# Performance work log

Measured on AMD Instinct MI355X. Metric: run time of the kernel, lower is better.

The kernel has to match this reference:

```python
import jax, jax.numpy as jnp
import numpy as np

B, S, T = 32, 512, 20      # sentences, tokens/sentence, chars/word
N_CHARS = 128              # embedding rows = N_CHARS + 1 (0 is pad)
D = 128                    # char_dim
H = 256                    # char_lstm_dim


def _gru_last_state(x_tnd, mask_tn, Wk, Wr, b):
    """Keras GRU (reset_after=True, gate order z,r,h) over time-major input.
    x_tnd: [T, N, D], mask_tn: [T, N] bool. Masked steps pass state through.
    Returns final hidden state [N, H]."""
    h_dim = Wr.shape[0]
    b_in, b_rec = b[0], b[1]

    def step(h, inp):
        x, m = inp
        xg = x @ Wk + b_in            # [N, 3H]
        hg = h @ Wr + b_rec           # [N, 3H]
        xz, xr, xh = jnp.split(xg, 3, axis=-1)
        hz, hr, hh = jnp.split(hg, 3, axis=-1)
        z = jax.nn.sigmoid(xz + hz)
        r = jax.nn.sigmoid(xr + hr)
        hc = jnp.tanh(xh + r * hh)
        hn = z * h + (1.0 - z) * hc
        hn = jnp.where(m[:, None], hn, h)
        return hn, None

    h0 = jnp.zeros((x_tnd.shape[1], h_dim), dtype=x_tnd.dtype)
    hT, _ = jax.lax.scan(step, h0, (x_tnd, mask_tn))
    return hT


def setup_inputs() -> dict:
    key = jax.random.key(0)
    ks = jax.random.split(key, 8)
    inputs = jax.random.randint(ks[0], (B, S, T), 0, N_CHARS + 1, dtype=jnp.int32)
    sc = 0.05
    emb = jax.random.normal(ks[1], (N_CHARS + 1, D), dtype=jnp.float32) * sc
    Wk_f = jax.random.normal(ks[2], (D, 3 * H), dtype=jnp.float32) * sc
    Wr_f = jax.random.normal(ks[3], (H, 3 * H), dtype=jnp.float32) * sc
    b_f = jnp.zeros((2, 3 * H), dtype=jnp.float32)
    Wk_b = jax.random.normal(ks[4], (D, 3 * H), dtype=jnp.float32) * sc
    Wr_b = jax.random.normal(ks[5], (H, 3 * H), dtype=jnp.float32) * sc
    b_b = jnp.zeros((2, 3 * H), dtype=jnp.float32)
    return {"inputs": inputs, "emb": emb, "Wk_f": Wk_f, "Wr_f": Wr_f,
            "b_f": b_f, "Wk_b": Wk_b, "Wr_b": Wr_b, "b_b": b_b}


def reference(inputs, emb, Wk_f, Wr_f, b_f, Wk_b, Wr_b, b_b):
    bsz, seq, wlen = inputs.shape
    h_dim = Wr_f.shape[0]
    flat = inputs.reshape(bsz * seq, wlen)           # [N, T]
    mask = flat != 0                                 # [N, T] (0 = pad)
    x = emb[flat]                                    # [N, T, D]
    x_t = jnp.transpose(x, (1, 0, 2))                # [T, N, D]
    m_t = mask.T                                     # [T, N]
    h_fwd = _gru_last_state(x_t, m_t, Wk_f, Wr_f, b_f)
    # Bidirectional: backward layer sees the reversed sequence + reversed mask
    h_bwd = _gru_last_state(x_t[::-1], m_t[::-1], Wk_b, Wr_b, b_b)
    out = jnp.concatenate([h_fwd, h_bwd], axis=-1)   # [N, 2H]
    return out.reshape(bsz, seq, 2 * h_dim)
```

## Files before the change

kernel.cpp:

```cpp
#include <hip/hip_runtime.h>
#include <hip/hip_bf16.h>

#define TS 20
#define DNUM 128
#define NWORDS 16384
#define NBLK 256

typedef __attribute__((ext_vector_type(8))) short s8v;
typedef __attribute__((ext_vector_type(4))) float f4v;

#define L2E 1.4426950408889634f

__device__ __forceinline__ unsigned short bf16_rne(float f) {
  union { float f; unsigned u; } x; x.f = f;
  unsigned r = x.u + 0x7fffu + ((x.u >> 16) & 1u);
  return (unsigned short)(r >> 16);
}

__global__ void build_tab(const float* __restrict__ emb,
                          const float* __restrict__ wkF, const float* __restrict__ bF,
                          const float* __restrict__ wkB, const float* __restrict__ bB,
                          float* __restrict__ tab2, float* __restrict__ tabh) {
  int gid = blockIdx.x * 256 + threadIdx.x;
  if (gid >= 2 * 129 * 768) return;
  int dir = gid / (129 * 768);
  int rem = gid - dir * (129 * 768);
  int c = rem / 768, j = rem - (rem / 768) * 768;
  int g = j >> 8, u = j & 255;
  const float* Wk = dir ? wkB : wkF;
  const float* bb = dir ? bB : bF;
  float s = bb[j];
  const float* er = emb + c * DNUM;
  #pragma unroll 4
  for (int d = 0; d < DNUM; ++d) s = fmaf(er[d], Wk[d * 768 + j], s);
  if (g < 2) tab2[(((size_t)dir * 129 + c) * 256 + u) * 2 + g] = -L2E * (s + bb[768 + j]);
  else       tabh[((size_t)dir * 129 + c) * 256 + u] = 2.f * L2E * s;
}

__global__ void pack_wr(const float* __restrict__ wrF, const float* __restrict__ wrB,
                        uint4* __restrict__ wp) {
  int gid = blockIdx.x * 256 + threadIdx.x;
  if (gid >= 2 * 48 * 8 * 64) return;
  int dir = gid / (48 * 8 * 64);
  int rem = gid - dir * (48 * 8 * 64);
  int ct = rem / (8 * 64);
  int kk = (rem / 64) & 7;
  int lane = rem & 63;
  const float* Wr = dir ? wrB : wrF;
  int n = ct * 16 + (lane & 15);
  int k0 = kk * 32 + (lane >> 4) * 8;
  const float sc = (ct >> 4) == 2 ? (2.f * L2E) : (-L2E);
  union { unsigned short v[8]; uint4 q; } u;
  #pragma unroll
  for (int e = 0; e < 8; ++e) u.v[e] = bf16_rne(sc * Wr[(k0 + e) * 768 + n]);
  wp[gid] = u.q;
}

__global__ __launch_bounds__(512, 2) void gru_main(
    const int* __restrict__ chars, const float* __restrict__ tab2,
    const float* __restrict__ tabh, const uint4* __restrict__ wrp,
    const float* __restrict__ bf_, const float* __restrict__ bb_,
    float* __restrict__ out) {
  const int bid = blockIdx.x;
  const int dir = bid >> 7;
  const int wslot = bid & 127;
  const float2* T2 = (const float2*)tab2 + (size_t)dir * 129 * 256;
  const float*  TH = tabh + (size_t)dir * 129 * 256;
  const uint4* WP = wrp + dir * (48 * 8 * 64);
  const float* brec = (dir ? bb_ : bf_) + 768;

  const int tid = threadIdx.x;
  const int w = tid >> 6, lane = tid & 63;
  const int lr = lane >> 4, lc = lane & 15;
  const int u0 = w * 32 + lc, u1 = u0 + 16;

  __shared__ uint4 bhl[8192];
  __shared__ unsigned short hbf[16][264];
  __shared__ int sch[16 * TS];

  for (int i = tid; i < 8192; i += 512) bhl[i] = WP[16384 + i];

  uint4 Wz[2][8], Wrr[2][8];
  #pragma unroll
  for (int ct = 0; ct < 2; ++ct)
    #pragma unroll
    for (int kk = 0; kk < 8; ++kk) {
      Wz[ct][kk]  = WP[((w * 2 + ct) * 8 + kk) * 64 + lane];
      Wrr[ct][kk] = WP[((16 + w * 2 + ct) * 8 + kk) * 64 + lane];
    }

  float brh[2];
  brh[0] = 2.f * L2E * brec[512 + u0];
  brh[1] = 2.f * L2E * brec[512 + u1];

  #pragma unroll 1
  for (int grp = 0; grp < 8; ++grp) {
    const int word0 = wslot * 128 + grp * 16;

    for (int i = tid; i < 16 * 264 / 2; i += 512) ((unsigned*)&hbf[0][0])[i] = 0;
    for (int i = tid; i < 16 * TS; i += 512) sch[i] = chars[word0 * TS + i];

    float h[2][4];
    #pragma unroll
    for (int ct = 0; ct < 2; ++ct)
      #pragma unroll
      for (int r = 0; r < 4; ++r) h[ct][r] = 0.f;

    __syncthreads();

    #pragma unroll 1
    for (int t = 0; t < TS; ++t) {
      const int ts = dir ? (TS - 1 - t) : t;

      int cc[4];
      #pragma unroll
      for (int r = 0; r < 4; ++r) cc[r] = sch[(lr * 4 + r) * TS + ts];
      float2 p[2][4];
      float  q[2][4];
      #pragma unroll
      for (int ct = 0; ct < 2; ++ct)
        #pragma unroll
        for (int r = 0; r < 4; ++r) {
          const int off = cc[r] * 256 + (ct ? u1 : u0);
          p[ct][r] = T2[off];
          q[ct][r] = TH[off];
        }

      f4v az[2], ar[2], ah[2];
      #pragma unroll
      for (int ct = 0; ct < 2; ++ct) {
        az[ct] = f4v{0.f, 0.f, 0.f, 0.f};
        ar[ct] = az[ct];
        ah[ct] = f4v{brh[ct], brh[ct], brh[ct], brh[ct]};
      }
      #pragma unroll
      for (int kk = 0; kk < 8; ++kk) {
        const s8v aa = __builtin_bit_cast(s8v, *(const uint4*)&hbf[lc][kk * 32 + lr * 8]);
        #pragma unroll
        for (int ct = 0; ct < 2; ++ct) {
          const uint4 bh = bhl[((w * 2 + ct) * 8 + kk) * 64 + lane];
          az[ct] = __builtin_amdgcn_mfma_f32_16x16x32_bf16(aa, __builtin_bit_cast(s8v, Wz[ct][kk]),  az[ct], 0, 0, 0);
          ar[ct] = __builtin_amdgcn_mfma_f32_16x16x32_bf16(aa, __builtin_bit_cast(s8v, Wrr[ct][kk]), ar[ct], 0, 0, 0);
          ah[ct] = __builtin_amdgcn_mfma_f32_16x16x32_bf16(aa, __builtin_bit_cast(s8v, bh),          ah[ct], 0, 0, 0);
        }
      }
      __syncthreads();

      #pragma unroll
      for (int ct = 0; ct < 2; ++ct)
        #pragma unroll
        for (int r = 0; r < 4; ++r) {
          const float z  = __builtin_amdgcn_rcpf(1.f + __builtin_amdgcn_exp2f(p[ct][r].x + az[ct][r]));
          const float rr = __builtin_amdgcn_rcpf(1.f + __builtin_amdgcn_exp2f(p[ct][r].y + ar[ct][r]));
          const float hc = fmaf(-2.f, __builtin_amdgcn_rcpf(
              1.f + __builtin_amdgcn_exp2f(fmaf(rr, ah[ct][r], q[ct][r]))), 1.f);
          const float hp = h[ct][r];
          float hn = fmaf(1.f - z, hc - hp, hp);
          hn = (cc[r] != 0) ? hn : hp;
          h[ct][r] = hn;
          hbf[lr * 4 + r][ct ? u1 : u0] = bf16_rne(hn);
        }
      __syncthreads();
    }

    #pragma unroll
    for (int ct = 0; ct < 2; ++ct)
      #pragma unroll
      for (int r = 0; r < 4; ++r)
        out[(size_t)(word0 + lr * 4 + r) * 512 + dir * 256 + (ct ? u1 : u0)] = h[ct][r];
    __syncthreads();
  }
}

extern "C" void kernel_launch(void* const* d_in, const int* in_sizes, int n_in,
                              void* d_out, int out_size, void* d_ws, size_t ws_size,
                              hipStream_t stream) {
  const int* chars = (const int*)d_in[0];
  const float* emb = (const float*)d_in[1];
  const float* wkF = (const float*)d_in[2];
  const float* wrF = (const float*)d_in[3];
  const float* bF  = (const float*)d_in[4];
  const float* wkB = (const float*)d_in[5];
  const float* wrB = (const float*)d_in[6];
  const float* bB  = (const float*)d_in[7];
  float* outp = (float*)d_out;

  float* tab2 = (float*)d_ws;
  float* tabh = (float*)((char*)d_ws + 528384);
  uint4* wrp  = (uint4*)((char*)d_ws + 528384 + 264192);

  build_tab<<<(2 * 129 * 768 + 255) / 256, 256, 0, stream>>>(emb, wkF, bF, wkB, bB, tab2, tabh);
  pack_wr<<<(2 * 48 * 8 * 64 + 255) / 256, 256, 0, stream>>>(wrF, wrB, wrp);
  gru_main<<<NBLK, 512, 0, stream>>>(chars, tab2, tabh, wrp, bF, bB, outp);
}
```

Before: 321.7 us.

## Interleave two independent 16-word groups to overlap MFMA with gate epilogue

Each block now handles two independent 16-word batches at once, A and B, and staggers them. The MFMA recurrent matmul for one batch is issued while the transcendental gate epilogue of the other runs. This aims to hide the serial dependency latency of the recurrence and halves the number of outer group iterations. It costs more registers for the doubled accumulators and state under launch_bounds(512,2), which risks spills. The tanh-table load is also moved into the epilogue.

```diff
diff --git a/kernel.cpp b/kernel.cpp
--- a/kernel.cpp
+++ b/kernel.cpp
@@ -56,6 +56,62 @@
   wp[gid] = u.q;
 }
 
+#define GATHER_M(cc_, p_, RO_, ts_) do {                                      \
+  _Pragma("unroll")                                                           \
+  for (int r = 0; r < 4; ++r) cc_[r] = sch[(RO_ + lr * 4 + r) * TS + (ts_)];  \
+  _Pragma("unroll")                                                           \
+  for (int ct = 0; ct < 2; ++ct) {                                            \
+    _Pragma("unroll")                                                         \
+    for (int r = 0; r < 4; ++r)                                               \
+      p_[ct][r] = T2[cc_[r] * 256 + (ct ? u1 : u0)];                          \
+  }                                                                           \
+} while (0)
+
+#define MFMA_M(az_, ar_, ah_, RO_) do {                                       \
+  _Pragma("unroll")                                                           \
+  for (int ct = 0; ct < 2; ++ct) {                                            \
+    az_[ct] = f4v{0.f, 0.f, 0.f, 0.f};                                        \
+    ar_[ct] = az_[ct];                                                        \
+    ah_[ct] = f4v{brh[ct], brh[ct], brh[ct], brh[ct]};                        \
+  }                                                                           \
+  _Pragma("unroll")                                                           \
+  for (int kk = 0; kk < 8; ++kk) {                                            \
+    const s8v aa = __builtin_bit_cast(s8v,                                    \
+        *(const uint4*)&hbf[RO_ + lc][kk * 32 + lr * 8]);                     \
+    _Pragma("unroll")                                                         \
+    for (int ct = 0; ct < 2; ++ct) {                                          \
+      const uint4 bh = bhl[((w * 2 + ct) * 8 + kk) * 64 + lane];              \
+      az_[ct] = __builtin_amdgcn_mfma_f32_16x16x32_bf16(aa,                   \
+          __builtin_bit_cast(s8v, Wz[ct][kk]),  az_[ct], 0, 0, 0);            \
+      ar_[ct] = __builtin_amdgcn_mfma_f32_16x16x32_bf16(aa,                   \
+          __builtin_bit_cast(s8v, Wrr[ct][kk]), ar_[ct], 0, 0, 0);            \
+      ah_[ct] = __builtin_amdgcn_mfma_f32_16x16x32_bf16(aa,                   \
+          __builtin_bit_cast(s8v, bh),          ah_[ct], 0, 0, 0);            \
+    }                                                                         \
+  }                                                                           \
+} while (0)
+
+#define EPI_M(cc_, p_, az_, ar_, ah_, h_, RO_) do {                           \
+  _Pragma("unroll")                                                           \
+  for (int ct = 0; ct < 2; ++ct) {                                            \
+    _Pragma("unroll")                                                         \
+    for (int r = 0; r < 4; ++r) {                                             \
+      const float q = TH[cc_[r] * 256 + (ct ? u1 : u0)];                      \
+      const float z  = __builtin_amdgcn_rcpf(                                 \
+          1.f + __builtin_amdgcn_exp2f(p_[ct][r].x + az_[ct][r]));            \
+      const float rr = __builtin_amdgcn_rcpf(                                 \
+          1.f + __builtin_amdgcn_exp2f(p_[ct][r].y + ar_[ct][r]));            \
+      const float hc = fmaf(-2.f, __builtin_amdgcn_rcpf(                      \
+          1.f + __builtin_amdgcn_exp2f(fmaf(rr, ah_[ct][r], q))), 1.f);       \
+      const float hp = h_[ct][r];                                             \
+      float hn = fmaf(1.f - z, hc - hp, hp);                                  \
+      hn = (cc_[r] != 0) ? hn : hp;                                           \
+      h_[ct][r] = hn;                                                         \
+      hbf[RO_ + lr * 4 + r][ct ? u1 : u0] = bf16_rne(hn);                     \
+    }                                                                         \
+  }                                                                           \
+} while (0)
+
 __global__ __launch_bounds__(512, 2) void gru_main(
     const int* __restrict__ chars, const float* __restrict__ tab2,
     const float* __restrict__ tabh, const uint4* __restrict__ wrp,
@@ -75,8 +131,8 @@
   const int u0 = w * 32 + lc, u1 = u0 + 16;
 
   __shared__ uint4 bhl[8192];
-  __shared__ unsigned short hbf[16][264];
-  __shared__ int sch[16 * TS];
+  __shared__ unsigned short hbf[32][264];
+  __shared__ int sch[32 * TS];
 
   for (int i = tid; i < 8192; i += 512) bhl[i] = WP[16384 + i];
 
@@ -94,81 +150,59 @@
   brh[1] = 2.f * L2E * brec[512 + u1];
 
   #pragma unroll 1
-  for (int grp = 0; grp < 8; ++grp) {
-    const int word0 = wslot * 128 + grp * 16;
-
-    for (int i = tid; i < 16 * 264 / 2; i += 512) ((unsigned*)&hbf[0][0])[i] = 0;
-    for (int i = tid; i < 16 * TS; i += 512) sch[i] = chars[word0 * TS + i];
-
-    float h[2][4];
+  for (int big = 0; big < 4; ++big) {
+    const int word0 = wslot * 128 + big * 32;
+
+    __syncthreads();
+    for (int i = tid; i < 32 * 264 / 2; i += 512) ((unsigned*)&hbf[0][0])[i] = 0;
+    for (int i = tid; i < 32 * TS; i += 512) sch[i] = chars[word0 * TS + i];
+
+    float hA[2][4], hB[2][4];
     #pragma unroll
     for (int ct = 0; ct < 2; ++ct)
       #pragma unroll
-      for (int r = 0; r < 4; ++r) h[ct][r] = 0.f;
-
+      for (int r = 0; r < 4; ++r) { hA[ct][r] = 0.f; hB[ct][r] = 0.f; }
+
+    __syncthreads();
+
+    int ccA[4], ccB[4];
+    float2 pA[2][4], pB[2][4];
+    f4v azA[2], arA[2], ahA[2], azB[2], arB[2], ahB[2];
+
+    {
+      const int ts0 = dir ? (TS - 1) : 0;
+      GATHER_M(ccA, pA, 0, ts0);
+      MFMA_M(azA, arA, ahA, 0);
+    }
     __syncthreads();
 
     #pragma unroll 1
     for (int t = 0; t < TS; ++t) {
       const int ts = dir ? (TS - 1 - t) : t;
 
-      int cc[4];
-      #pragma unroll
-      for (int r = 0; r < 4; ++r) cc[r] = sch[(lr * 4 + r) * TS + ts];
-      float2 p[2][4];
-      float  q[2][4];
-      #pragma unroll
-      for (int ct = 0; ct < 2; ++ct)
-        #pragma unroll
-        for (int r = 0; r < 4; ++r) {
-          const int off = cc[r] * 256 + (ct ? u1 : u0);
-          p[ct][r] = T2[off];
-          q[ct][r] = TH[off];
-        }
-
-      f4v az[2], ar[2], ah[2];
-      #pragma unroll
-      for (int ct = 0; ct < 2; ++ct) {
-        az[ct] = f4v{0.f, 0.f, 0.f, 0.f};
-        ar[ct] = az[ct];
-        ah[ct] = f4v{brh[ct], brh[ct], brh[ct], brh[ct]};
+      GATHER_M(ccB, pB, 16, ts);
+      MFMA_M(azB, arB, ahB, 16);
+      EPI_M(ccA, pA, azA, arA, ahA, hA, 0);
+      __syncthreads();
+
+      if (t < TS - 1) {
+        const int ts2 = dir ? (TS - 2 - t) : (t + 1);
+        GATHER_M(ccA, pA, 0, ts2);
+        MFMA_M(azA, arA, ahA, 0);
+        EPI_M(ccB, pB, azB, arB, ahB, hB, 16);
+        __syncthreads();
+      } else {
+        EPI_M(ccB, pB, azB, arB, ahB, hB, 16);
       }
-      #pragma unroll
-      for (int kk = 0; kk < 8; ++kk) {
-        const s8v aa = __builtin_bit_cast(s8v, *(const uint4*)&hbf[lc][kk * 32 + lr * 8]);
-        #pragma unroll
-        for (int ct = 0; ct < 2; ++ct) {
-          const uint4 bh = bhl[((w * 2 + ct) * 8 + kk) * 64 + lane];
-          az[ct] = __builtin_amdgcn_mfma_f32_16x16x32_bf16(aa, __builtin_bit_cast(s8v, Wz[ct][kk]),  az[ct], 0, 0, 0);
-          ar[ct] = __builtin_amdgcn_mfma_f32_16x16x32_bf16(aa, __builtin_bit_cast(s8v, Wrr[ct][kk]), ar[ct], 0, 0, 0);
-          ah[ct] = __builtin_amdgcn_mfma_f32_16x16x32_bf16(aa, __builtin_bit_cast(s8v, bh),          ah[ct], 0, 0, 0);
-        }
-      }
-      __syncthreads();
-
-      #pragma unroll
-      for (int ct = 0; ct < 2; ++ct)
-        #pragma unroll
-        for (int r = 0; r < 4; ++r) {
-          const float z  = __builtin_amdgcn_rcpf(1.f + __builtin_amdgcn_exp2f(p[ct][r].x + az[ct][r]));
-          const float rr = __builtin_amdgcn_rcpf(1.f + __builtin_amdgcn_exp2f(p[ct][r].y + ar[ct][r]));
-          const float hc = fmaf(-2.f, __builtin_amdgcn_rcpf(
-              1.f + __builtin_amdgcn_exp2f(fmaf(rr, ah[ct][r], q[ct][r]))), 1.f);
-          const float hp = h[ct][r];
-          float hn = fmaf(1.f - z, hc - hp, hp);
-          hn = (cc[r] != 0) ? hn : hp;
-          h[ct][r] = hn;
-          hbf[lr * 4 + r][ct ? u1 : u0] = bf16_rne(hn);
-        }
-      __syncthreads();
     }
 
     #pragma unroll
     for (int ct = 0; ct < 2; ++ct)
       #pragma unroll
-      for (int r = 0; r < 4; ++r)
-        out[(size_t)(word0 + lr * 4 + r) * 512 + dir * 256 + (ct ? u1 : u0)] = h[ct][r];
-    __syncthreads();
+      for (int r = 0; r < 4; ++r) {
+        out[(size_t)(word0 + lr * 4 + r) * 512 + dir * 256 + (ct ? u1 : u0)] = hA[ct][r];
+        out[(size_t)(word0 + 16 + lr * 4 + r) * 512 + dir * 256 + (ct ? u1 : u0)] = hB[ct][r];
+      }
   }
 }
 
```

Result: slower. 916.2 us (+184.8%).

## Process two 16-word groups per step and pack gate tables into float4

Applied to the files above, without the earlier changes.

Each block now runs 32 words per time step as two independent 16-row MFMA tiles sharing the same weight fragments. This doubles the independent MFMA and transcendental work available between barriers and halves the number of serial group iterations. The input-gate tables are merged into one float4-per-unit layout so a single vector load fetches all three gates. Launch bounds drop to one block per CU to allow the extra registers, so per-CU occupancy falls in exchange for more instruction-level parallelism.

```diff
diff --git a/kernel.cpp b/kernel.cpp
--- a/kernel.cpp
+++ b/kernel.cpp
@@ -20,7 +20,7 @@
 __global__ void build_tab(const float* __restrict__ emb,
                           const float* __restrict__ wkF, const float* __restrict__ bF,
                           const float* __restrict__ wkB, const float* __restrict__ bB,
-                          float* __restrict__ tab2, float* __restrict__ tabh) {
+                          float* __restrict__ tab4) {
   int gid = blockIdx.x * 256 + threadIdx.x;
   if (gid >= 2 * 129 * 768) return;
   int dir = gid / (129 * 768);
@@ -33,8 +33,8 @@
   const float* er = emb + c * DNUM;
   #pragma unroll 4
   for (int d = 0; d < DNUM; ++d) s = fmaf(er[d], Wk[d * 768 + j], s);
-  if (g < 2) tab2[(((size_t)dir * 129 + c) * 256 + u) * 2 + g] = -L2E * (s + bb[768 + j]);
-  else       tabh[((size_t)dir * 129 + c) * 256 + u] = 2.f * L2E * s;
+  float v = (g < 2) ? (-L2E * (s + bb[768 + j])) : (2.f * L2E * s);
+  tab4[((((size_t)dir * 129 + c) * 256 + u) * 4) + g] = v;
 }
 
 __global__ void pack_wr(const float* __restrict__ wrF, const float* __restrict__ wrB,
@@ -56,16 +56,14 @@
   wp[gid] = u.q;
 }
 
-__global__ __launch_bounds__(512, 2) void gru_main(
-    const int* __restrict__ chars, const float* __restrict__ tab2,
-    const float* __restrict__ tabh, const uint4* __restrict__ wrp,
-    const float* __restrict__ bf_, const float* __restrict__ bb_,
-    float* __restrict__ out) {
+__global__ __launch_bounds__(512, 1) void gru_main(
+    const int* __restrict__ chars, const float* __restrict__ tab4,
+    const uint4* __restrict__ wrp, const float* __restrict__ bf_,
+    const float* __restrict__ bb_, float* __restrict__ out) {
   const int bid = blockIdx.x;
   const int dir = bid >> 7;
   const int wslot = bid & 127;
-  const float2* T2 = (const float2*)tab2 + (size_t)dir * 129 * 256;
-  const float*  TH = tabh + (size_t)dir * 129 * 256;
+  const float4* T4 = (const float4*)tab4 + (size_t)dir * 129 * 256;
   const uint4* WP = wrp + dir * (48 * 8 * 64);
   const float* brec = (dir ? bb_ : bf_) + 768;
 
@@ -75,8 +73,8 @@
   const int u0 = w * 32 + lc, u1 = u0 + 16;
 
   __shared__ uint4 bhl[8192];
-  __shared__ unsigned short hbf[16][264];
-  __shared__ int sch[16 * TS];
+  __shared__ unsigned short hbf[32][264];
+  __shared__ int sch[32 * TS];
 
   for (int i = tid; i < 8192; i += 512) bhl[i] = WP[16384 + i];
 
@@ -94,17 +92,17 @@
   brh[1] = 2.f * L2E * brec[512 + u1];
 
   #pragma unroll 1
-  for (int grp = 0; grp < 8; ++grp) {
-    const int word0 = wslot * 128 + grp * 16;
-
-    for (int i = tid; i < 16 * 264 / 2; i += 512) ((unsigned*)&hbf[0][0])[i] = 0;
-    for (int i = tid; i < 16 * TS; i += 512) sch[i] = chars[word0 * TS + i];
-
-    float h[2][4];
+  for (int grp = 0; grp < 4; ++grp) {
+    const int word0 = wslot * 128 + grp * 32;
+
+    for (int i = tid; i < 32 * 264 / 2; i += 512) ((unsigned*)&hbf[0][0])[i] = 0;
+    for (int i = tid; i < 32 * TS; i += 512) sch[i] = chars[word0 * TS + i];
+
+    float hA[2][4], hB[2][4];
     #pragma unroll
     for (int ct = 0; ct < 2; ++ct)
       #pragma unroll
-      for (int r = 0; r < 4; ++r) h[ct][r] = 0.f;
+      for (int r = 0; r < 4; ++r) { hA[ct][r] = 0.f; hB[ct][r] = 0.f; }
 
     __syncthreads();
 
@@ -112,53 +110,84 @@
     for (int t = 0; t < TS; ++t) {
       const int ts = dir ? (TS - 1 - t) : t;
 
-      int cc[4];
-      #pragma unroll
-      for (int r = 0; r < 4; ++r) cc[r] = sch[(lr * 4 + r) * TS + ts];
-      float2 p[2][4];
-      float  q[2][4];
+      int ccA[4], ccB[4];
+      #pragma unroll
+      for (int r = 0; r < 4; ++r) {
+        ccA[r] = sch[(lr * 4 + r) * TS + ts];
+        ccB[r] = sch[(16 + lr * 4 + r) * TS + ts];
+      }
+      float4 gA[2][4];
+      #pragma unroll
+      for (int ct = 0; ct < 2; ++ct)
+        #pragma unroll
+        for (int r = 0; r < 4; ++r)
+          gA[ct][r] = T4[ccA[r] * 256 + (ct ? u1 : u0)];
+
+      f4v azA[2], arA[2], ahA[2], azB[2], arB[2], ahB[2];
+      #pragma unroll
+      for (int ct = 0; ct < 2; ++ct) {
+        azA[ct] = f4v{0.f, 0.f, 0.f, 0.f};
+        arA[ct] = azA[ct];
+        ahA[ct] = f4v{brh[ct], brh[ct], brh[ct], brh[ct]};
+        azB[ct] = azA[ct];
+        arB[ct] = azA[ct];
+        ahB[ct] = ahA[ct];
+      }
+      #pragma unroll
+      for (int kk = 0; kk < 8; ++kk) {
+        const s8v aaA = __builtin_bit_cast(s8v, *(const uint4*)&hbf[lc][kk * 32 + lr * 8]);
+        const s8v aaB = __builtin_bit_cast(s8v, *(const uint4*)&hbf[16 + lc][kk * 32 + lr * 8]);
+        #pragma unroll
+        for (int ct = 0; ct < 2; ++ct) {
+          const s8v bz = __builtin_bit_cast(s8v, Wz[ct][kk]);
+          const s8v br = __builtin_bit_cast(s8v, Wrr[ct][kk]);
+          const s8v bh = __builtin_bit_cast(s8v, bhl[((w * 2 + ct) * 8 + kk) * 64 + lane]);
+          azA[ct] = __builtin_amdgcn_mfma_f32_16x16x32_bf16(aaA, bz, azA[ct], 0, 0, 0);
+          arA[ct] = __builtin_amdgcn_mfma_f32_16x16x32_bf16(aaA, br, arA[ct], 0, 0, 0);
+          ahA[ct] = __builtin_amdgcn_mfma_f32_16x16x32_bf16(aaA, bh, ahA[ct], 0, 0, 0);
+          azB[ct] = __builtin_amdgcn_mfma_f32_16x16x32_bf16(aaB, bz, azB[ct], 0, 0, 0);
+          arB[ct] = __builtin_amdgcn_mfma_f32_16x16x32_bf16(aaB, br, arB[ct], 0, 0, 0);
+          ahB[ct] = __builtin_amdgcn_mfma_f32_16x16x32_bf16(aaB, bh, ahB[ct], 0, 0, 0);
+        }
+      }
+      __syncthreads();
+
+      float4 gB[2][4];
+      #pragma unroll
+      for (int ct = 0; ct < 2; ++ct)
+        #pragma unroll
+        for (int r = 0; r < 4; ++r)
+          gB[ct][r] = T4[ccB[r] * 256 + (ct ? u1 : u0)];
+
       #pragma unroll
       for (int ct = 0; ct < 2; ++ct)
         #pragma unroll
         for (int r = 0; r < 4; ++r) {
-          const int off = cc[r] * 256 + (ct ? u1 : u0);
-          p[ct][r] = T2[off];
-          q[ct][r] = TH[off];
+          const float4 g = gA[ct][r];
+          const float z  = __builtin_amdgcn_rcpf(1.f + __builtin_amdgcn_exp2f(g.x + azA[ct][r]));
+          const float rr = __builtin_amdgcn_rcpf(1.f + __builtin_amdgcn_exp2f(g.y + arA[ct][r]));
+          const float hc = fmaf(-2.f, __builtin_amdgcn_rcpf(
+              1.f + __builtin_amdgcn_exp2f(fmaf(rr, ahA[ct][r], g.z))), 1.f);
+          const float hp = hA[ct][r];
+          float hn = fmaf(1.f - z, hc - hp, hp);
+          hn = (ccA[r] != 0) ? hn : hp;
+          hA[ct][r] = hn;
+          hbf[lr * 4 + r][ct ? u1 : u0] = bf16_rne(hn);
         }
-
-      f4v az[2], ar[2], ah[2];
-      #pragma unroll
-      for (int ct = 0; ct < 2; ++ct) {
-        az[ct] = f4v{0.f, 0.f, 0.f, 0.f};
-        ar[ct] = az[ct];
-        ah[ct] = f4v{brh[ct], brh[ct], brh[ct], brh[ct]};
-      }
-      #pragma unroll
-      for (int kk = 0; kk < 8; ++kk) {
-        const s8v aa = __builtin_bit_cast(s8v, *(const uint4*)&hbf[lc][kk * 32 + lr * 8]);
-        #pragma unroll
-        for (int ct = 0; ct < 2; ++ct) {
-          const uint4 bh = bhl[((w * 2 + ct) * 8 + kk) * 64 + lane];
-          az[ct] = __builtin_amdgcn_mfma_f32_16x16x32_bf16(aa, __builtin_bit_cast(s8v, Wz[ct][kk]),  az[ct], 0, 0, 0);
-          ar[ct] = __builtin_amdgcn_mfma_f32_16x16x32_bf16(aa, __builtin_bit_cast(s8v, Wrr[ct][kk]), ar[ct], 0, 0, 0);
-          ah[ct] = __builtin_amdgcn_mfma_f32_16x16x32_bf16(aa, __builtin_bit_cast(s8v, bh),          ah[ct], 0, 0, 0);
-        }
-      }
-      __syncthreads();
-
       #pragma unroll
       for (int ct = 0; ct < 2; ++ct)
         #pragma unroll
         for (int r = 0; r < 4; ++r) {
-          const float z  = __builtin_amdgcn_rcpf(1.f + __builtin_amdgcn_exp2f(p[ct][r].x + az[ct][r]));
-          const float rr = __builtin_amdgcn_rcpf(1.f + __builtin_amdgcn_exp2f(p[ct][r].y + ar[ct][r]));
+          const float4 g = gB[ct][r];
+          const float z  = __builtin_amdgcn_rcpf(1.f + __builtin_amdgcn_exp2f(g.x + azB[ct][r]));
+          const float rr = __builtin_amdgcn_rcpf(1.f + __builtin_amdgcn_exp2f(g.y + arB[ct][r]));
           const float hc = fmaf(-2.f, __builtin_amdgcn_rcpf(
-              1.f + __builtin_amdgcn_exp2f(fmaf(rr, ah[ct][r], q[ct][r]))), 1.f);
-          const float hp = h[ct][r];
+              1.f + __builtin_amdgcn_exp2f(fmaf(rr, ahB[ct][r], g.z))), 1.f);
+          const float hp = hB[ct][r];
           float hn = fmaf(1.f - z, hc - hp, hp);
-          hn = (cc[r] != 0) ? hn : hp;
-          h[ct][r] = hn;
-          hbf[lr * 4 + r][ct ? u1 : u0] = bf16_rne(hn);
+          hn = (ccB[r] != 0) ? hn : hp;
+          hB[ct][r] = hn;
+          hbf[16 + lr * 4 + r][ct ? u1 : u0] = bf16_rne(hn);
         }
       __syncthreads();
     }
@@ -166,8 +195,10 @@
     #pragma unroll
     for (int ct = 0; ct < 2; ++ct)
       #pragma unroll
-      for (int r = 0; r < 4; ++r)
-        out[(size_t)(word0 + lr * 4 + r) * 512 + dir * 256 + (ct ? u1 : u0)] = h[ct][r];
+      for (int r = 0; r < 4; ++r) {
+        out[(size_t)(word0 + lr * 4 + r) * 512 + dir * 256 + (ct ? u1 : u0)] = hA[ct][r];
+        out[(size_t)(word0 + 16 + lr * 4 + r) * 512 + dir * 256 + (ct ? u1 : u0)] = hB[ct][r];
+      }
     __syncthreads();
   }
 }
@@ -185,11 +216,10 @@
   const float* bB  = (const float*)d_in[7];
   float* outp = (float*)d_out;
 
-  float* tab2 = (float*)d_ws;
-  float* tabh = (float*)((char*)d_ws + 528384);
-  uint4* wrp  = (uint4*)((char*)d_ws + 528384 + 264192);
-
-  build_tab<<<(2 * 129 * 768 + 255) / 256, 256, 0, stream>>>(emb, wkF, bF, wkB, bB, tab2, tabh);
+  float* tab4 = (float*)d_ws;
+  uint4* wrp  = (uint4*)((char*)d_ws + 1056768);
+
+  build_tab<<<(2 * 129 * 768 + 255) / 256, 256, 0, stream>>>(emb, wkF, bF, wkB, bB, tab4);
   pack_wr<<<(2 * 48 * 8 * 64 + 255) / 256, 256, 0, stream>>>(wrF, wrB, wrp);
-  gru_main<<<NBLK, 512, 0, stream>>>(chars, tab2, tabh, wrp, bF, bB, outp);
-}
+  gru_main<<<NBLK, 512, 0, stream>>>(chars, tab4, wrp, bF, bB, outp);
+}
```

After: 352.1 us. +9.4%, slower.
